# Kernel optimization log

Hardware: AMD Instinct MI355X
Metric: run time of the kernel (lower is better)

The kernel has to match this reference:

```python
import jax, jax.numpy as jnp
import numpy as np

B, N, C = 2, 384, 11            # images, proposals/img, classes (incl background)
RCN = 5                          # (xc, yc, w, h, angle_deg)
WEIGHTS = (10.0, 10.0, 5.0, 5.0, 1.0)
SCORE_THRESH = 0.05
NMS_THRESH = 0.5
DET_PER_IMG = 100
BBOX_XFORM_CLIP = float(np.log(1000.0 / 16.0))
EPS = 1e-8


def setup_inputs() -> dict:
    key = jax.random.key(0)
    k1, k2, k3, k4, k5 = jax.random.split(key, 5)
    class_logits = jax.random.normal(k1, (B * N, C), jnp.float32) * 2.0
    box_regression = jax.random.normal(k2, (B * N, C * RCN), jnp.float32) * 0.5
    xy = jax.random.uniform(k3, (B * N, 2), jnp.float32, 0.0, 1024.0)
    wh = jax.random.uniform(k4, (B * N, 2), jnp.float32, 16.0, 256.0)
    ang = jax.random.uniform(k5, (B * N, 1), jnp.float32, -90.0, 90.0)
    rrects = jnp.concatenate([xy, wh, ang], -1)
    return {"class_logits": class_logits, "box_regression": box_regression, "rrects": rrects}


def cross2(a, b):
    return a[..., 0] * b[..., 1] - a[..., 1] * b[..., 0]


def decode(rel, anchors):
    # rel (...,5) deltas, anchors (...,5) rotated boxes; relative angle coder
    wx, wy, ww, wh, wa = WEIGHTS
    dx = rel[..., 0] / wx
    dy = rel[..., 1] / wy
    dw = jnp.clip(rel[..., 2] / ww, None, BBOX_XFORM_CLIP)
    dh = jnp.clip(rel[..., 3] / wh, None, BBOX_XFORM_CLIP)
    da = rel[..., 4] / wa
    xc, yc, w, h, a = (anchors[..., i] for i in range(5))
    px = dx * w + xc
    py = dy * h + yc
    pw = jnp.exp(dw) * w
    ph = jnp.exp(dh) * h
    pa = da * (180.0 / np.pi) + a
    pa = (pa + 180.0) % 360.0 - 180.0
    return jnp.stack([px, py, pw, ph, pa], -1)


def corners(b):
    # (...,5) -> (...,4,2) rectangle corners (CCW in box frame)
    xc, yc, w, h, a = (b[..., i] for i in range(5))
    t = a * (np.pi / 180.0)
    c, s = jnp.cos(t), jnp.sin(t)
    hx, hy = w * 0.5, h * 0.5
    lx = jnp.stack([-hx, hx, hx, -hx], -1)
    ly = jnp.stack([-hy, -hy, hy, hy], -1)
    px = xc[..., None] + lx * c[..., None] - ly * s[..., None]
    py = yc[..., None] + lx * s[..., None] + ly * c[..., None]
    return jnp.stack([px, py], -1)


def inter_area(ca, cb):
    # intersection area of two convex quads (4,2),(4,2): candidate points =
    # 16 edge-edge intersections + 8 contained corners, sorted by angle, shoelace
    a0, b0 = ca, cb
    d1 = jnp.roll(ca, -1, 0) - ca
    d2 = jnp.roll(cb, -1, 0) - cb
    den = cross2(d1[:, None, :], d2[None, :, :])                # (4,4)
    diff = b0[None, :, :] - a0[:, None, :]
    den_s = jnp.where(jnp.abs(den) < EPS, 1.0, den)
    t = cross2(diff, d2[None, :, :]) / den_s
    u = cross2(diff, d1[:, None, :]) / den_s
    ok = (jnp.abs(den) >= EPS) & (t >= 0) & (t <= 1) & (u >= 0) & (u <= 1)
    pint = a0[:, None, :] + t[..., None] * d1[:, None, :]       # (4,4,2)

    def inside(p, cs):
        ev = jnp.roll(cs, -1, 0) - cs
        cr = cross2(ev[None, :, :], p[:, None, :] - cs[None, :, :])  # (4,4)
        return jnp.all(cr >= -1e-6, -1) | jnp.all(cr <= 1e-6, -1)

    pts = jnp.concatenate([pint.reshape(16, 2), ca, cb], 0)     # (24,2)
    msk = jnp.concatenate([ok.reshape(16), inside(ca, cb), inside(cb, ca)], 0)
    nv = jnp.sum(msk)
    cen = jnp.sum(pts * msk[:, None], 0) / jnp.maximum(nv, 1)
    pts = jnp.where(msk[:, None], pts, cen)                     # park invalid at centroid
    ang = jnp.arctan2(pts[:, 1] - cen[1], pts[:, 0] - cen[0])
    p = pts[jnp.argsort(ang)]
    area = 0.5 * jnp.abs(jnp.sum(cross2(p, jnp.roll(p, -1, 0))))
    return jnp.where(nv >= 3, area, 0.0)


def rotated_iou_matrix(boxes):
    # boxes (N,5) -> (N,N) rotated IoU
    cs = corners(boxes)
    area = boxes[:, 2] * boxes[:, 3]
    inter = jax.vmap(lambda ci: jax.vmap(lambda cj: inter_area(ci, cj))(cs))(cs)
    return inter / (area[:, None] + area[None, :] - inter + EPS)


def greedy_nms(iou, scores, valid):
    n = iou.shape[0]
    order = jnp.argsort(-jnp.where(valid, scores, -jnp.inf))
    ios = iou[order][:, order]
    vs = valid[order]
    idx = jnp.arange(n)

    def body(i, sup):
        cur_ok = (~sup[i]) & vs[i]
        return sup | (cur_ok & (ios[i] > NMS_THRESH) & (idx > i))

    sup = jax.lax.fori_loop(0, n, body, jnp.zeros((n,), bool))
    keep_sorted = (~sup) & vs
    return jnp.zeros((n,), bool).at[order].set(keep_sorted)


def reference(class_logits, box_regression, rrects):
    prob = jax.nn.softmax(class_logits, -1)                     # (M,C)
    rel = box_regression.reshape(B * N, C, RCN)
    dec = decode(rel, rrects[:, None, :])                       # (M,C,5)
    boxes = dec.reshape(B, N, C, RCN)
    scores = prob.reshape(B, N, C)
    fg_boxes = jnp.moveaxis(boxes[:, :, 1:, :], 2, 1)           # (B,C-1,N,5)
    fg_scores = jnp.moveaxis(scores[:, :, 1:], 2, 1)            # (B,C-1,N)
    valid = fg_scores > SCORE_THRESH
    iou = jax.vmap(jax.vmap(rotated_iou_matrix))(fg_boxes)      # (B,C-1,N,N)
    keep = jax.vmap(jax.vmap(greedy_nms))(iou, fg_scores, valid)
    flat_scores = jnp.where(keep, fg_scores, -1.0).reshape(B, (C - 1) * N)
    top_s, top_i = jax.lax.top_k(flat_scores, DET_PER_IMG)
    sel_boxes = jnp.take_along_axis(fg_boxes.reshape(B, (C - 1) * N, RCN), top_i[:, :, None], axis=1)
    labels = top_i // N + 1
    ok = top_s > 0.0
    out = jnp.concatenate([jnp.where(ok[..., None], sel_boxes, 0.0), jnp.where(ok, top_s, 0.0)[..., None]], -1)
    labels = jnp.where(ok, labels, 0)
    return out, labels
```

## Files before the change

kernel.cpp:

```cpp
#include <hip/hip_runtime.h>
#include <cmath>

#define NPROP 384
#define NB 2
#define NCLS 11
#define NFG 10
#define BC_TOTAL (NB*NFG)
#define M_TOTAL (NB*NPROP)
#define FLAT_PER_IMG (NFG*NPROP)
#define DET 100
#define PAIR_LDS_CAP 6144

#define OFF_BOXES 0
#define OFF_KIDX  38400
#define OFF_KSC   46080
#define OFF_KCNT  53760

typedef unsigned long long ull;

__device__ __forceinline__ void mk_corners(float px, float py, float pw, float ph, float pa,
                                           float cxo[4], float cyo[4]) {
    float t = pa * 0.017453292519943295f;
    float ct = cosf(t), st = sinf(t);
    float hx = pw*0.5f, hy = ph*0.5f;
    float lx[4] = {-hx, hx, hx, -hx};
    float ly[4] = {-hy, -hy, hy, hy};
#pragma unroll
    for (int k = 0; k < 4; ++k) {
        cxo[k] = px + lx[k]*ct - ly[k]*st;
        cyo[k] = py + lx[k]*st + ly[k]*ct;
    }
}

__device__ float inter_area_net(const float ax[4], const float ay[4],
                                const float bx[4], const float by[4]) {
    float d1x[4], d1y[4], d2x[4], d2y[4];
#pragma unroll
    for (int k = 0; k < 4; ++k) {
        int k1 = (k + 1) & 3;
        d1x[k] = ax[k1] - ax[k]; d1y[k] = ay[k1] - ay[k];
        d2x[k] = bx[k1] - bx[k]; d2y[k] = by[k1] - by[k];
    }
    float ex[32], ey[32];
    bool msk[24];
#pragma unroll
    for (int i = 0; i < 4; ++i) {
#pragma unroll
        for (int j = 0; j < 4; ++j) {
            float den = d1x[i]*d2y[j] - d1y[i]*d2x[j];
            float dfx = bx[j]-ax[i], dfy = by[j]-ay[i];
            float dens = (fabsf(den) < 1e-8f) ? 1.0f : den;
            float t = (dfx*d2y[j] - dfy*d2x[j]) / dens;
            float u = (dfx*d1y[i] - dfy*d1x[i]) / dens;
            bool ok = (fabsf(den) >= 1e-8f) && t >= 0.0f && t <= 1.0f
                                            && u >= 0.0f && u <= 1.0f;
            ex[i*4+j] = ax[i] + t*d1x[i];
            ey[i*4+j] = ay[i] + t*d1y[i];
            msk[i*4+j] = ok;
        }
    }
#pragma unroll
    for (int i = 0; i < 4; ++i) {
        bool allp = true, alln = true;
#pragma unroll
        for (int j = 0; j < 4; ++j) {
            float cr = d2x[j]*(ay[i]-by[j]) - d2y[j]*(ax[i]-bx[j]);
            allp = allp && (cr >= -1e-6f);
            alln = alln && (cr <= 1e-6f);
        }
        ex[16+i] = ax[i]; ey[16+i] = ay[i]; msk[16+i] = allp || alln;
    }
#pragma unroll
    for (int i = 0; i < 4; ++i) {
        bool allp = true, alln = true;
#pragma unroll
        for (int j = 0; j < 4; ++j) {
            float cr = d1x[j]*(by[i]-ay[j]) - d1y[j]*(bx[i]-ax[j]);
            allp = allp && (cr >= -1e-6f);
            alln = alln && (cr <= 1e-6f);
        }
        ex[20+i] = bx[i]; ey[20+i] = by[i]; msk[20+i] = allp || alln;
    }
    int nv = 0; float sx = 0.f, sy = 0.f;
#pragma unroll
    for (int k = 0; k < 24; ++k)
        if (msk[k]) { nv++; sx += ex[k]; sy += ey[k]; }
    float fm = (float)(nv > 1 ? nv : 1);
    float cx = sx / fm, cy = sy / fm;
    unsigned key[32];
#pragma unroll
    for (int k = 0; k < 24; ++k) {
        float qx = msk[k] ? ex[k] : cx;
        float qy = msk[k] ? ey[k] : cy;
        ex[k] = qx; ey[k] = qy;
        float dx = qx - cx, dy = qy - cy;
        float den = fabsf(dx) + fabsf(dy);
        float r = (den > 0.0f) ? dy / den : 0.0f;
        float p = (dx >= 0.0f) ? r : ((dy >= 0.0f) ? 2.0f - r : -2.0f - r);
        p = p + 0.0f;
        unsigned u = __float_as_uint(p);
        u = (u & 0x80000000u) ? ~u : (u | 0x80000000u);
        key[k] = (u & 0xFFFFFFE0u) | (unsigned)k;
    }
#pragma unroll
    for (int k = 24; k < 32; ++k) { key[k] = 0xFFFFFFFFu; ex[k] = 0.f; ey[k] = 0.f; }
#pragma unroll
    for (int k = 2; k <= 32; k <<= 1) {
#pragma unroll
        for (int j = k >> 1; j > 0; j >>= 1) {
#pragma unroll
            for (int i = 0; i < 32; ++i) {
                int l = i ^ j;
                if (l > i) {
                    bool up = ((i & k) == 0);
                    unsigned ka = key[i], kb = key[l];
                    bool sw = up ? (ka > kb) : (ka < kb);
                    float xa = ex[i], xb = ex[l];
                    float ya = ey[i], yb = ey[l];
                    key[i] = sw ? kb : ka; key[l] = sw ? ka : kb;
                    ex[i]  = sw ? xb : xa; ex[l]  = sw ? xa : xb;
                    ey[i]  = sw ? yb : ya; ey[l]  = sw ? ya : yb;
                }
            }
        }
    }
    float s = 0.f;
#pragma unroll
    for (int k = 0; k < 24; ++k) {
        int n = (k + 1 == 24) ? 0 : (k + 1);
        s += ex[k]*ey[n] - ey[k]*ex[n];
    }
    float area = 0.5f * fabsf(s);
    return (nv >= 3) ? area : 0.0f;
}

__device__ __forceinline__ void eval_pair_lds(const float* pxL, const float* pyL,
                                              const float* pwL, const float* phL,
                                              const float* paL, const float* areaL,
                                              ull* supL, int hi, int lo) {
    float axp[4], ayp[4], bxp[4], byp[4];
    mk_corners(pxL[hi], pyL[hi], pwL[hi], phL[hi], paL[hi], axp, ayp);
    mk_corners(pxL[lo], pyL[lo], pwL[lo], phL[lo], paL[lo], bxp, byp);
    float inter = inter_area_net(axp, ayp, bxp, byp);
    float iou = inter / (areaL[hi] + areaL[lo] - inter + 1e-8f);
    if (iou > 0.5f)
        atomicOr((unsigned int*)supL + hi*12 + (lo >> 5), 1u << (lo & 31));
}

__global__ __launch_bounds__(384)
void bc_kernel(const float* __restrict__ logits,
               const float* __restrict__ boxreg,
               const float* __restrict__ rrects,
               float* __restrict__ ws,
               float* __restrict__ out) {
    __shared__ float pxL[NPROP], pyL[NPROP], pwL[NPROP], phL[NPROP], paL[NPROP];
    __shared__ float areaL[NPROP], scoreL[NPROP], radL[NPROP];
    __shared__ int   origL[NPROP];
    __shared__ ull   supL[NPROP*6];
    __shared__ unsigned pairL[PAIR_LDS_CAP];
    __shared__ ull   keyL[NPROP];
    __shared__ int   orderL[NPROP];
    __shared__ unsigned char keepS[NPROP];
    __shared__ int   wcntS[8];
    __shared__ int   cntS, pcntS;

    int bc = blockIdx.x, t = threadIdx.x;
    int b = bc / NFG, cls = (bc % NFG) + 1;
    int wv = t >> 6, lane = t & 63;

    int gq = bc*NPROP + t;
    if (gq < NB*DET*6 + NB*DET) out[gq] = 0.0f;
    if (t == 0) { cntS = 0; pcntS = 0; }
    keepS[t] = 0;
    for (int k = t; k < NPROP*6; k += NPROP) supL[k] = 0ull;
    {
        int m = b*NPROP + t;
        float lg[NCLS];
        float mx = -INFINITY;
#pragma unroll
        for (int c = 0; c < NCLS; ++c) { lg[c] = logits[m*NCLS+c]; mx = fmaxf(mx, lg[c]); }
        float sum = 0.f;
#pragma unroll
        for (int c = 0; c < NCLS; ++c) sum += expf(lg[c]-mx);
        float prob = expf(lg[cls]-mx) / sum;
        float axc = rrects[m*5+0], ayc = rrects[m*5+1];
        float aw  = rrects[m*5+2], ah  = rrects[m*5+3], aa = rrects[m*5+4];
        const float* rel = boxreg + m*(NCLS*5) + cls*5;
        float dx = rel[0] / 10.0f;
        float dy = rel[1] / 10.0f;
        float dw = fminf(rel[2] / 5.0f, 4.1351665567423205f);
        float dh = fminf(rel[3] / 5.0f, 4.1351665567423205f);
        float da = rel[4];
        float px = dx*aw + axc;
        float py = dy*ah + ayc;
        float pw = expf(dw)*aw;
        float ph = expf(dh)*ah;
        float pa = da*57.29577951308232f + aa;
        float xm = pa + 180.0f;
        float r = fmodf(xm, 360.0f);
        if (r < 0.0f) r += 360.0f;
        pa = r - 180.0f;
        pxL[t]=px; pyL[t]=py; pwL[t]=pw; phL[t]=ph; paL[t]=pa;
        areaL[t]=pw*ph; scoreL[t]=prob;
        radL[t]=0.5f*sqrtf(pw*pw + ph*ph);
        float* boxes = ws + OFF_BOXES;
        int o = bc*NPROP + t;
        boxes[o*5+0]=px; boxes[o*5+1]=py; boxes[o*5+2]=pw; boxes[o*5+3]=ph; boxes[o*5+4]=pa;
        bool vi = prob > 0.05f;
        keyL[t] = vi ? (((ull)__float_as_uint(prob) << 32) | (ull)(0xFFFFFFFFu - (unsigned)t))
                     : (ull)(0xFFFFFFFFu - (unsigned)t);
    }
    __syncthreads();

    if (scoreL[t] > 0.05f) {
        int p = atomicAdd(&cntS, 1);
        origL[p] = t;
    }
    {
        ull myk = keyL[t];
        int r = 0;
        for (int k = 0; k < NPROP; k += 8) {
            int acc = 0;
#pragma unroll
            for (int q = 0; q < 8; ++q) acc += (keyL[k+q] > myk) ? 1 : 0;
            r += acc;
        }
        orderL[r] = t;
    }
    __syncthreads();
    int cnt = cntS;

    for (int a = wv; a < cnt; a += 6) {
        int ia = origL[a];
        float cxa = pxL[ia], cya = pyL[ia], ra = radL[ia], Aa = areaL[ia], sa = scoreL[ia];
        for (int b0 = a + 1; b0 < cnt; b0 += 64) {
            int bb = b0 + lane;
            bool go = false; int ib = 0;
            if (bb < cnt) {
                ib = origL[bb];
                float ddx = cxa - pxL[ib], ddy = cya - pyL[ib];
                float rr = ra + radL[ib];
                go = (ddx*ddx + ddy*ddy <= rr*rr);
                float Ab = areaL[ib];
                float mn = fminf(Aa, Ab);
                go = go && (3.0f*mn > Aa + Ab);
            }
            if (go) {
                float sb = scoreL[ib];
                bool afirst = (sa > sb) || (sa == sb && ia < ib);
                int hi = afirst ? ia : ib;
                int lo = afirst ? ib : ia;
                int pos = atomicAdd(&pcntS, 1);
                if (pos < PAIR_LDS_CAP)
                    pairL[pos] = ((unsigned)hi << 16) | (unsigned)lo;
                else
                    eval_pair_lds(pxL, pyL, pwL, phL, paL, areaL, supL, hi, lo);
            }
        }
    }
    __syncthreads();

    {
        int np = pcntS; if (np > PAIR_LDS_CAP) np = PAIR_LDS_CAP;
        for (int p = t; p < np; p += NPROP) {
            unsigned pk = pairL[p];
            eval_pair_lds(pxL, pyL, pwL, phL, paL, areaL, supL,
                          (int)(pk >> 16), (int)(pk & 0xFFFFu));
        }
    }
    __syncthreads();

    if (t < 64) {
        int NV = cnt;
        int ord0 = orderL[lane],      ord1 = orderL[64+lane];
        int ord2 = orderL[128+lane],  ord3 = orderL[192+lane];
        int ord4 = orderL[256+lane],  ord5 = orderL[320+lane];
        ull mask = 0ull;
        int o_cur = __shfl(ord0, 0);
        ull row_cur = (lane < 6) ? supL[o_cur*6 + lane] : 0ull;
        for (int p = 0; p < NV; ++p) {
            int pn = (p + 1 < NPROP) ? (p + 1) : 0;
            int seg = pn >> 6, sl = pn & 63;
            int on = __shfl(ord0, sl);
            on = (seg == 1) ? __shfl(ord1, sl) : on;
            on = (seg == 2) ? __shfl(ord2, sl) : on;
            on = (seg == 3) ? __shfl(ord3, sl) : on;
            on = (seg == 4) ? __shfl(ord4, sl) : on;
            on = (seg == 5) ? __shfl(ord5, sl) : on;
            ull row_next = (lane < 6) ? supL[on*6 + lane] : 0ull;
            bool myhit = (lane == (o_cur >> 6)) && ((mask >> (o_cur & 63)) & 1ull);
            ull bal = __ballot(myhit);
            if (bal == 0ull) {
                if (lane == 0) keepS[o_cur] = 1;
                mask |= row_cur;
            }
            row_cur = row_next;
            o_cur = on;
        }
    }
    __syncthreads();

    bool kp = keepS[t] != 0;
    ull bal = __ballot(kp);
    if (lane == 0) wcntS[wv] = __popcll(bal);
    __syncthreads();
    if (t == 0) {
        int s = 0;
#pragma unroll
        for (int w = 0; w < 6; ++w) { int c = wcntS[w]; wcntS[w] = s; s += c; }
        ((unsigned int*)(ws + OFF_KCNT))[bc] = (unsigned)s;
    }
    __syncthreads();
    if (kp) {
        int pos = wcntS[wv] + (int)__popcll(bal & ((1ull << lane) - 1ull));
        ((unsigned int*)(ws + OFF_KIDX))[bc*NPROP + pos] = (unsigned)((bc % NFG)*NPROP + t);
        (ws + OFF_KSC)[bc*NPROP + pos] = scoreL[t];
    }
}

__global__ __launch_bounds__(256)
void topk_kernel(const float* __restrict__ ws, float* __restrict__ out) {
    __shared__ ull keyL[FLAT_PER_IMG];
    int b = blockIdx.x >> 4;
    int slice = blockIdx.x & 15;
    int t = threadIdx.x;
    const unsigned int* kidx2 = (const unsigned int*)(ws + OFF_KIDX);
    const float* ksc2 = ws + OFF_KSC;
    const unsigned int* kcnt2 = (const unsigned int*)(ws + OFF_KCNT);
    const float* boxes = ws + OFF_BOXES;
    int offs[NFG], cnts[NFG];
    int K = 0;
#pragma unroll
    for (int fg = 0; fg < NFG; ++fg) {
        cnts[fg] = (int)kcnt2[b*NFG + fg];
        offs[fg] = K;
        K += cnts[fg];
    }
#pragma unroll
    for (int fg = 0; fg < NFG; ++fg) {
        int bc = b*NFG + fg;
        for (int k = t; k < cnts[fg]; k += 256) {
            unsigned sb = __float_as_uint(ksc2[bc*NPROP + k]);
            unsigned f  = kidx2[bc*NPROP + k];
            keyL[offs[fg] + k] = ((ull)sb << 32) | (ull)(0xFFFFFFFFu - f);
        }
    }
    int KP = (K + 15) & ~15;
    for (int k = K + t; k < KP; k += 256) keyL[k] = 0ull;
    __syncthreads();
    int e = slice*256 + t;
    if (e >= K) return;
    ull my = keyL[e];
    int r = 0;
    for (int k = 0; k < KP; k += 16) {
        int acc = 0;
#pragma unroll
        for (int q = 0; q < 16; ++q)
            acc += (keyL[k+q] > my) ? 1 : 0;
        r += acc;
    }
    if (r < DET) {
        unsigned f = 0xFFFFFFFFu - (unsigned)(my & 0xFFFFFFFFu);
        float s = __uint_as_float((unsigned)(my >> 32));
        int src = b*FLAT_PER_IMG + (int)f;
        float* row = out + (b*DET + r)*6;
#pragma unroll
        for (int q = 0; q < 5; ++q) row[q] = boxes[src*5+q];
        row[5] = s;
        out[NB*DET*6 + b*DET + r] = (float)(f / NPROP + 1);
    }
}

extern "C" void kernel_launch(void* const* d_in, const int* in_sizes, int n_in,
                              void* d_out, int out_size, void* d_ws, size_t ws_size,
                              hipStream_t stream) {
    const float* logits = (const float*)d_in[0];
    const float* boxreg = (const float*)d_in[1];
    const float* rrects = (const float*)d_in[2];
    float* out = (float*)d_out;
    float* ws  = (float*)d_ws;
    (void)in_sizes; (void)n_in; (void)out_size; (void)ws_size;

    bc_kernel<<<BC_TOTAL, NPROP, 0, stream>>>(logits, boxreg, rrects, ws, out);
    topk_kernel<<<NB * 16, 256, 0, stream>>>(ws, out);
}
```

Measured before the change: 142.8 us.

## Split fused kernel into pairgen, parallel pair-IoU, and NMS kernels

The single per-class kernel (20 blocks) is split into three kernels. Pair generation writes candidate pairs to global memory, the expensive rotated-IoU evaluation runs across 320 blocks, and a separate NMS kernel reads the suppression bitmask back from global. Pair slot allocation also moves to one atomic per wave with a ballot prefix, replacing one atomic per pair. This spreads the heavy IoU work over far more CUs than the 20-block launch. The cost is two extra launches plus global-memory traffic and global atomics for boxes and the bitmask.

```diff
diff --git a/kernel.cpp b/kernel.cpp
--- a/kernel.cpp
+++ b/kernel.cpp
@@ -9,12 +9,17 @@
 #define M_TOTAL (NB*NPROP)
 #define FLAT_PER_IMG (NFG*NPROP)
 #define DET 100
-#define PAIR_LDS_CAP 6144
+#define PAIR_SLICE 3072
 
 #define OFF_BOXES 0
-#define OFF_KIDX  38400
-#define OFF_KSC   46080
-#define OFF_KCNT  53760
+#define OFF_AREA  38400
+#define OFF_SCORE 46080
+#define OFF_SUP   53760
+#define OFF_KIDX  145920
+#define OFF_KSC   153600
+#define OFF_KCNT  161280
+#define OFF_PCNT  161312
+#define OFF_PAIRS 161344
 
 typedef unsigned long long ull;
 
@@ -134,45 +139,44 @@
     return (nv >= 3) ? area : 0.0f;
 }
 
-__device__ __forceinline__ void eval_pair_lds(const float* pxL, const float* pyL,
-                                              const float* pwL, const float* phL,
-                                              const float* paL, const float* areaL,
-                                              ull* supL, int hi, int lo) {
+__device__ __forceinline__ void eval_pair_glob(float* ws, int bc, int hi, int lo) {
+    const float* boxes = ws + OFF_BOXES;
+    const float* areaA = ws + OFF_AREA;
+    unsigned int* supw = (unsigned int*)(ws + OFF_SUP);
+    int rowi = bc*NPROP + hi, rowj = bc*NPROP + lo;
     float axp[4], ayp[4], bxp[4], byp[4];
-    mk_corners(pxL[hi], pyL[hi], pwL[hi], phL[hi], paL[hi], axp, ayp);
-    mk_corners(pxL[lo], pyL[lo], pwL[lo], phL[lo], paL[lo], bxp, byp);
+    mk_corners(boxes[rowi*5+0], boxes[rowi*5+1], boxes[rowi*5+2],
+               boxes[rowi*5+3], boxes[rowi*5+4], axp, ayp);
+    mk_corners(boxes[rowj*5+0], boxes[rowj*5+1], boxes[rowj*5+2],
+               boxes[rowj*5+3], boxes[rowj*5+4], bxp, byp);
     float inter = inter_area_net(axp, ayp, bxp, byp);
-    float iou = inter / (areaL[hi] + areaL[lo] - inter + 1e-8f);
+    float iou = inter / (areaA[rowi] + areaA[rowj] - inter + 1e-8f);
     if (iou > 0.5f)
-        atomicOr((unsigned int*)supL + hi*12 + (lo >> 5), 1u << (lo & 31));
+        atomicOr(&supw[rowi*12 + (lo >> 5)], 1u << (lo & 31));
 }
 
 __global__ __launch_bounds__(384)
-void bc_kernel(const float* __restrict__ logits,
-               const float* __restrict__ boxreg,
-               const float* __restrict__ rrects,
-               float* __restrict__ ws,
-               float* __restrict__ out) {
-    __shared__ float pxL[NPROP], pyL[NPROP], pwL[NPROP], phL[NPROP], paL[NPROP];
-    __shared__ float areaL[NPROP], scoreL[NPROP], radL[NPROP];
+void pairgen_kernel(const float* __restrict__ logits,
+                    const float* __restrict__ boxreg,
+                    const float* __restrict__ rrects,
+                    float* __restrict__ ws,
+                    float* __restrict__ out) {
+    __shared__ float pxL[NPROP], pyL[NPROP], radL[NPROP], areaL[NPROP], scoreL[NPROP];
     __shared__ int   origL[NPROP];
-    __shared__ ull   supL[NPROP*6];
-    __shared__ unsigned pairL[PAIR_LDS_CAP];
-    __shared__ ull   keyL[NPROP];
-    __shared__ int   orderL[NPROP];
-    __shared__ unsigned char keepS[NPROP];
-    __shared__ int   wcntS[8];
-    __shared__ int   cntS, pcntS;
-
+    __shared__ int   wbase[8];
+    __shared__ int   pcntS;
     int bc = blockIdx.x, t = threadIdx.x;
     int b = bc / NFG, cls = (bc % NFG) + 1;
     int wv = t >> 6, lane = t & 63;
 
     int gq = bc*NPROP + t;
     if (gq < NB*DET*6 + NB*DET) out[gq] = 0.0f;
-    if (t == 0) { cntS = 0; pcntS = 0; }
-    keepS[t] = 0;
-    for (int k = t; k < NPROP*6; k += NPROP) supL[k] = 0ull;
+    if (t == 0) pcntS = 0;
+    {
+        unsigned int* supw = (unsigned int*)(ws + OFF_SUP) + bc*NPROP*12;
+        for (int k = t; k < NPROP*12; k += NPROP) supw[k] = 0u;
+    }
+    float prob;
     {
         int m = b*NPROP + t;
         float lg[NCLS];
@@ -182,7 +186,7 @@
         float sum = 0.f;
 #pragma unroll
         for (int c = 0; c < NCLS; ++c) sum += expf(lg[c]-mx);
-        float prob = expf(lg[cls]-mx) / sum;
+        prob = expf(lg[cls]-mx) / sum;
         float axc = rrects[m*5+0], ayc = rrects[m*5+1];
         float aw  = rrects[m*5+2], ah  = rrects[m*5+3], aa = rrects[m*5+4];
         const float* rel = boxreg + m*(NCLS*5) + cls*5;
@@ -200,36 +204,30 @@
         float r = fmodf(xm, 360.0f);
         if (r < 0.0f) r += 360.0f;
         pa = r - 180.0f;
-        pxL[t]=px; pyL[t]=py; pwL[t]=pw; phL[t]=ph; paL[t]=pa;
-        areaL[t]=pw*ph; scoreL[t]=prob;
+        pxL[t]=px; pyL[t]=py; areaL[t]=pw*ph; scoreL[t]=prob;
         radL[t]=0.5f*sqrtf(pw*pw + ph*ph);
         float* boxes = ws + OFF_BOXES;
         int o = bc*NPROP + t;
         boxes[o*5+0]=px; boxes[o*5+1]=py; boxes[o*5+2]=pw; boxes[o*5+3]=ph; boxes[o*5+4]=pa;
-        bool vi = prob > 0.05f;
-        keyL[t] = vi ? (((ull)__float_as_uint(prob) << 32) | (ull)(0xFFFFFFFFu - (unsigned)t))
-                     : (ull)(0xFFFFFFFFu - (unsigned)t);
-    }
-    __syncthreads();
-
-    if (scoreL[t] > 0.05f) {
-        int p = atomicAdd(&cntS, 1);
-        origL[p] = t;
-    }
-    {
-        ull myk = keyL[t];
-        int r = 0;
-        for (int k = 0; k < NPROP; k += 8) {
-            int acc = 0;
-#pragma unroll
-            for (int q = 0; q < 8; ++q) acc += (keyL[k+q] > myk) ? 1 : 0;
-            r += acc;
-        }
-        orderL[r] = t;
-    }
-    __syncthreads();
-    int cnt = cntS;
-
+        ws[OFF_AREA + o]  = pw*ph;
+        ws[OFF_SCORE + o] = prob;
+    }
+    bool vi = prob > 0.05f;
+    ull vb = __ballot(vi);
+    if (lane == 0) wbase[wv] = __popcll(vb);
+    __syncthreads();
+    if (t == 0) {
+        int s = 0;
+#pragma unroll
+        for (int w = 0; w < 6; ++w) { int c = wbase[w]; wbase[w] = s; s += c; }
+        wbase[6] = s;
+    }
+    __syncthreads();
+    if (vi) origL[wbase[wv] + (int)__popcll(vb & ((1ull << lane) - 1ull))] = t;
+    __syncthreads();
+    int cnt = wbase[6];
+
+    unsigned int* pairs = (unsigned int*)(ws + OFF_PAIRS) + bc*PAIR_SLICE;
     for (int a = wv; a < cnt; a += 6) {
         int ia = origL[a];
         float cxa = pxL[ia], cya = pyL[ia], ra = radL[ia], Aa = areaL[ia], sa = scoreL[ia];
@@ -245,33 +243,74 @@
                 float mn = fminf(Aa, Ab);
                 go = go && (3.0f*mn > Aa + Ab);
             }
+            ull m = __ballot(go);
+            int base = 0;
+            if (lane == 0 && m) base = atomicAdd(&pcntS, __popcll(m));
+            base = __shfl(base, 0);
             if (go) {
                 float sb = scoreL[ib];
                 bool afirst = (sa > sb) || (sa == sb && ia < ib);
                 int hi = afirst ? ia : ib;
                 int lo = afirst ? ib : ia;
-                int pos = atomicAdd(&pcntS, 1);
-                if (pos < PAIR_LDS_CAP)
-                    pairL[pos] = ((unsigned)hi << 16) | (unsigned)lo;
+                int pos = base + (int)__popcll(m & ((1ull << lane) - 1ull));
+                if (pos < PAIR_SLICE)
+                    pairs[pos] = ((unsigned)hi << 10) | (unsigned)lo;
                 else
-                    eval_pair_lds(pxL, pyL, pwL, phL, paL, areaL, supL, hi, lo);
+                    eval_pair_glob(ws, bc, hi, lo);
             }
         }
     }
     __syncthreads();
-
+    if (t == 0) ((unsigned int*)(ws + OFF_PCNT))[bc] = (unsigned)pcntS;
+}
+
+__global__ __launch_bounds__(256)
+void heavy_kernel(float* __restrict__ ws) {
+    int bc = blockIdx.x >> 4;
+    int chunk = blockIdx.x & 15;
+    unsigned n = ((const unsigned int*)(ws + OFF_PCNT))[bc];
+    if (n > PAIR_SLICE) n = PAIR_SLICE;
+    const unsigned int* pairs = (const unsigned int*)(ws + OFF_PAIRS) + bc*PAIR_SLICE;
+    for (unsigned p = chunk*256u + threadIdx.x; p < n; p += 4096u) {
+        unsigned pk = pairs[p];
+        eval_pair_glob(ws, bc, (int)(pk >> 10), (int)(pk & 0x3FFu));
+    }
+}
+
+__global__ __launch_bounds__(384)
+void nms_kernel(float* __restrict__ ws) {
+    __shared__ ull keyL[NPROP];
+    __shared__ int orderL[NPROP];
+    __shared__ ull supL[NPROP*6];
+    __shared__ unsigned char keepS[NPROP];
+    __shared__ int wcntS[8];
+    int bc = blockIdx.x, t = threadIdx.x;
+    int wv = t >> 6, lane = t & 63;
+    const float* scoreA = ws + OFF_SCORE;
+    const ull* supG = (const ull*)(ws + OFF_SUP);
+    float sc = scoreA[bc*NPROP + t];
+    bool vi = sc > 0.05f;
+    ull myk = vi ? (((ull)__float_as_uint(sc) << 32) | (ull)(0xFFFFFFFFu - (unsigned)t))
+                 : (ull)(0xFFFFFFFFu - (unsigned)t);
+    keyL[t] = myk;
+    keepS[t] = 0;
+    ull vb = __ballot(vi);
+    if (lane == 0) wcntS[wv] = __popcll(vb);
+    __syncthreads();
     {
-        int np = pcntS; if (np > PAIR_LDS_CAP) np = PAIR_LDS_CAP;
-        for (int p = t; p < np; p += NPROP) {
-            unsigned pk = pairL[p];
-            eval_pair_lds(pxL, pyL, pwL, phL, paL, areaL, supL,
-                          (int)(pk >> 16), (int)(pk & 0xFFFFu));
-        }
-    }
-    __syncthreads();
-
+        int r = 0;
+        for (int k = 0; k < NPROP; k += 8) {
+            int acc = 0;
+#pragma unroll
+            for (int q = 0; q < 8; ++q) acc += (keyL[k+q] > myk) ? 1 : 0;
+            r += acc;
+        }
+        orderL[r] = t;
+    }
+    for (int k = t; k < NPROP*6; k += NPROP) supL[k] = supG[bc*NPROP*6 + k];
+    __syncthreads();
+    int NV = wcntS[0] + wcntS[1] + wcntS[2] + wcntS[3] + wcntS[4] + wcntS[5];
     if (t < 64) {
-        int NV = cnt;
         int ord0 = orderL[lane],      ord1 = orderL[64+lane];
         int ord2 = orderL[128+lane],  ord3 = orderL[192+lane];
         int ord4 = orderL[256+lane],  ord5 = orderL[320+lane];
@@ -299,7 +338,6 @@
         }
     }
     __syncthreads();
-
     bool kp = keepS[t] != 0;
     ull bal = __ballot(kp);
     if (lane == 0) wcntS[wv] = __popcll(bal);
@@ -314,7 +352,7 @@
     if (kp) {
         int pos = wcntS[wv] + (int)__popcll(bal & ((1ull << lane) - 1ull));
         ((unsigned int*)(ws + OFF_KIDX))[bc*NPROP + pos] = (unsigned)((bc % NFG)*NPROP + t);
-        (ws + OFF_KSC)[bc*NPROP + pos] = scoreL[t];
+        (ws + OFF_KSC)[bc*NPROP + pos] = sc;
     }
 }
 
@@ -381,6 +419,8 @@
     float* ws  = (float*)d_ws;
     (void)in_sizes; (void)n_in; (void)out_size; (void)ws_size;
 
-    bc_kernel<<<BC_TOTAL, NPROP, 0, stream>>>(logits, boxreg, rrects, ws, out);
+    pairgen_kernel<<<BC_TOTAL, NPROP, 0, stream>>>(logits, boxreg, rrects, ws, out);
+    heavy_kernel<<<BC_TOTAL * 16, 256, 0, stream>>>(ws);
+    nms_kernel<<<BC_TOTAL, NPROP, 0, stream>>>(ws);
     topk_kernel<<<NB * 16, 256, 0, stream>>>(ws, out);
 }
```

Result: no change. 143.2 us (+0.3%).

## Double block size to 768 threads and aggregate pair-list atomics per wave

Applied to the files above, without the earlier changes.

Launches the per-(image,class) kernel with 768 threads instead of 384, spreading the candidate-pair scan over 12 waves and the IoU evaluation over twice as many threads. Replaces per-lane LDS atomicAdd on the pair counter with one wave-level atomic plus a ballot prefix, and builds the compacted valid list with a deterministic ballot scan instead of atomics. The rank sort is moved after pair evaluation, and the LDS pair buffer shrinks to 4096 entries. More overflow pairs may fall back to the slower inline path, and the extra idle threads add sync cost.

```diff
diff --git a/kernel.cpp b/kernel.cpp
--- a/kernel.cpp
+++ b/kernel.cpp
@@ -6,10 +6,9 @@
 #define NCLS 11
 #define NFG 10
 #define BC_TOTAL (NB*NFG)
-#define M_TOTAL (NB*NPROP)
 #define FLAT_PER_IMG (NFG*NPROP)
 #define DET 100
-#define PAIR_LDS_CAP 6144
+#define PAIR_LDS_CAP 4096
 
 #define OFF_BOXES 0
 #define OFF_KIDX  38400
@@ -147,7 +146,7 @@
         atomicOr((unsigned int*)supL + hi*12 + (lo >> 5), 1u << (lo & 31));
 }
 
-__global__ __launch_bounds__(384)
+__global__ __launch_bounds__(768)
 void bc_kernel(const float* __restrict__ logits,
                const float* __restrict__ boxreg,
                const float* __restrict__ rrects,
@@ -156,24 +155,25 @@
     __shared__ float pxL[NPROP], pyL[NPROP], pwL[NPROP], phL[NPROP], paL[NPROP];
     __shared__ float areaL[NPROP], scoreL[NPROP], radL[NPROP];
     __shared__ int   origL[NPROP];
+    __shared__ unsigned pairL[PAIR_LDS_CAP];
     __shared__ ull   supL[NPROP*6];
-    __shared__ unsigned pairL[PAIR_LDS_CAP];
     __shared__ ull   keyL[NPROP];
     __shared__ int   orderL[NPROP];
     __shared__ unsigned char keepS[NPROP];
-    __shared__ int   wcntS[8];
-    __shared__ int   cntS, pcntS;
+    __shared__ int   wbase[16];
+    __shared__ int   totS, pcntS;
 
     int bc = blockIdx.x, t = threadIdx.x;
     int b = bc / NFG, cls = (bc % NFG) + 1;
     int wv = t >> 6, lane = t & 63;
 
-    int gq = bc*NPROP + t;
-    if (gq < NB*DET*6 + NB*DET) out[gq] = 0.0f;
-    if (t == 0) { cntS = 0; pcntS = 0; }
-    keepS[t] = 0;
-    for (int k = t; k < NPROP*6; k += NPROP) supL[k] = 0ull;
-    {
+    int g = bc*768 + t;
+    if (g < NB*DET*6 + NB*DET) out[g] = 0.0f;
+    if (t == 0) { pcntS = 0; }
+    for (int k = t; k < NPROP*6; k += 768) supL[k] = 0ull;
+
+    float prob = 0.0f;
+    if (t < NPROP) {
         int m = b*NPROP + t;
         float lg[NCLS];
         float mx = -INFINITY;
@@ -182,7 +182,7 @@
         float sum = 0.f;
 #pragma unroll
         for (int c = 0; c < NCLS; ++c) sum += expf(lg[c]-mx);
-        float prob = expf(lg[cls]-mx) / sum;
+        prob = expf(lg[cls]-mx) / sum;
         float axc = rrects[m*5+0], ayc = rrects[m*5+1];
         float aw  = rrects[m*5+2], ah  = rrects[m*5+3], aa = rrects[m*5+4];
         const float* rel = boxreg + m*(NCLS*5) + cls*5;
@@ -209,28 +209,24 @@
         bool vi = prob > 0.05f;
         keyL[t] = vi ? (((ull)__float_as_uint(prob) << 32) | (ull)(0xFFFFFFFFu - (unsigned)t))
                      : (ull)(0xFFFFFFFFu - (unsigned)t);
-    }
-    __syncthreads();
-
-    if (scoreL[t] > 0.05f) {
-        int p = atomicAdd(&cntS, 1);
-        origL[p] = t;
-    }
-    {
-        ull myk = keyL[t];
-        int r = 0;
-        for (int k = 0; k < NPROP; k += 8) {
-            int acc = 0;
-#pragma unroll
-            for (int q = 0; q < 8; ++q) acc += (keyL[k+q] > myk) ? 1 : 0;
-            r += acc;
-        }
-        orderL[r] = t;
-    }
-    __syncthreads();
-    int cnt = cntS;
-
-    for (int a = wv; a < cnt; a += 6) {
+        keepS[t] = 0;
+    }
+    bool vi = (t < NPROP) && (prob > 0.05f);
+    ull vb = __ballot(vi);
+    if (lane == 0) wbase[wv] = __popcll(vb);
+    __syncthreads();
+    if (t == 0) {
+        int s = 0;
+#pragma unroll
+        for (int w = 0; w < 6; ++w) { int c = wbase[w]; wbase[w] = s; s += c; }
+        totS = s;
+    }
+    __syncthreads();
+    if (vi) origL[wbase[wv] + (int)__popcll(vb & ((1ull << lane) - 1ull))] = t;
+    __syncthreads();
+    int cnt = totS;
+
+    for (int a = wv; a < cnt; a += 12) {
         int ia = origL[a];
         float cxa = pxL[ia], cya = pyL[ia], ra = radL[ia], Aa = areaL[ia], sa = scoreL[ia];
         for (int b0 = a + 1; b0 < cnt; b0 += 64) {
@@ -245,12 +241,16 @@
                 float mn = fminf(Aa, Ab);
                 go = go && (3.0f*mn > Aa + Ab);
             }
+            ull m = __ballot(go);
+            int base = 0;
+            if (lane == 0 && m) base = atomicAdd(&pcntS, __popcll(m));
+            base = __shfl(base, 0);
             if (go) {
                 float sb = scoreL[ib];
                 bool afirst = (sa > sb) || (sa == sb && ia < ib);
                 int hi = afirst ? ia : ib;
                 int lo = afirst ? ib : ia;
-                int pos = atomicAdd(&pcntS, 1);
+                int pos = base + (int)__popcll(m & ((1ull << lane) - 1ull));
                 if (pos < PAIR_LDS_CAP)
                     pairL[pos] = ((unsigned)hi << 16) | (unsigned)lo;
                 else
@@ -262,11 +262,24 @@
 
     {
         int np = pcntS; if (np > PAIR_LDS_CAP) np = PAIR_LDS_CAP;
-        for (int p = t; p < np; p += NPROP) {
+        for (int p = t; p < np; p += 768) {
             unsigned pk = pairL[p];
             eval_pair_lds(pxL, pyL, pwL, phL, paL, areaL, supL,
                           (int)(pk >> 16), (int)(pk & 0xFFFFu));
         }
+    }
+    __syncthreads();
+
+    if (t < NPROP) {
+        ull myk = keyL[t];
+        int r = 0;
+        for (int k = 0; k < NPROP; k += 8) {
+            int acc = 0;
+#pragma unroll
+            for (int q = 0; q < 8; ++q) acc += (keyL[k+q] > myk) ? 1 : 0;
+            r += acc;
+        }
+        orderL[r] = t;
     }
     __syncthreads();
 
@@ -300,19 +313,19 @@
     }
     __syncthreads();
 
-    bool kp = keepS[t] != 0;
+    bool kp = (t < NPROP) && (keepS[t] != 0);
     ull bal = __ballot(kp);
-    if (lane == 0) wcntS[wv] = __popcll(bal);
+    if (lane == 0) wbase[wv] = __popcll(bal);
     __syncthreads();
     if (t == 0) {
         int s = 0;
 #pragma unroll
-        for (int w = 0; w < 6; ++w) { int c = wcntS[w]; wcntS[w] = s; s += c; }
+        for (int w = 0; w < 6; ++w) { int c = wbase[w]; wbase[w] = s; s += c; }
         ((unsigned int*)(ws + OFF_KCNT))[bc] = (unsigned)s;
     }
     __syncthreads();
     if (kp) {
-        int pos = wcntS[wv] + (int)__popcll(bal & ((1ull << lane) - 1ull));
+        int pos = wbase[wv] + (int)__popcll(bal & ((1ull << lane) - 1ull));
         ((unsigned int*)(ws + OFF_KIDX))[bc*NPROP + pos] = (unsigned)((bc % NFG)*NPROP + t);
         (ws + OFF_KSC)[bc*NPROP + pos] = scoreL[t];
     }
@@ -381,6 +394,6 @@
     float* ws  = (float*)d_ws;
     (void)in_sizes; (void)n_in; (void)out_size; (void)ws_size;
 
-    bc_kernel<<<BC_TOTAL, NPROP, 0, stream>>>(logits, boxreg, rrects, ws, out);
+    bc_kernel<<<BC_TOTAL, 768, 0, stream>>>(logits, boxreg, rrects, ws, out);
     topk_kernel<<<NB * 16, 256, 0, stream>>>(ws, out);
 }
```

Result: slower. 149.0 us (+4.4%).
